# Kernel optimization log

Hardware: AMD Instinct MI355X
Metric: run time of the kernel (lower is better)

Reference implementation:

```python
import jax, jax.numpy as jnp
import numpy as np

L, HID, NH, NKV, HD, INTER = 16, 960, 15, 5, 64, 2560
VOCAB, NV, NT, PRE, SD = 49152, 192, 48, 241, 32
THETA, EPS, B = 100000.0, 1e-5, 16
GROUPS = NH // NKV


def setup_inputs() -> dict:
    key = jax.random.key(0)
    ks = jax.random.split(key, 20)
    s = 0.02
    rn = lambda k, shp: jax.random.normal(k, shp, jnp.float32) * s
    return {
        'vision_features': jax.random.normal(ks[0], (B, NV, HID), jnp.float32),
        'lang_token_ids': jax.random.randint(ks[1], (B, NT), 0, VOCAB),
        'lang_mask': jnp.ones((B, NT), dtype=bool),
        'state': jax.random.normal(ks[2], (B, SD), jnp.float32),
        'embed': rn(ks[3], (VOCAB, HID)),
        'state_w': rn(ks[4], (SD, HID)),
        'state_b': jnp.zeros((HID,), jnp.float32),
        'Wq': rn(ks[5], (L, HID, NH * HD)),
        'Wk': rn(ks[6], (L, HID, NKV * HD)),
        'Wv': rn(ks[7], (L, HID, NKV * HD)),
        'Wo': rn(ks[8], (L, NH * HD, HID)),
        'Wg': rn(ks[9], (L, HID, INTER)),
        'Wu': rn(ks[10], (L, HID, INTER)),
        'Wd': rn(ks[11], (L, INTER, HID)),
        'ln1': jnp.ones((L, HID), jnp.float32),
        'ln2': jnp.ones((L, HID), jnp.float32),
    }


def _rms(x, w):
    var = jnp.mean(jnp.square(x), axis=-1, keepdims=True)
    return x * jax.lax.rsqrt(var + EPS) * w


def _rotate_half(x):
    h = x.shape[-1] // 2
    return jnp.concatenate([-x[..., h:], x[..., :h]], axis=-1)


def _rope_tables(position_ids):
    # position_ids: [B, S] -> cos/sin: [B, S, HD]
    inv_freq = 1.0 / (THETA ** (jnp.arange(0, HD, 2, dtype=jnp.float32) / HD))
    freqs = position_ids.astype(jnp.float32)[..., None] * inv_freq  # [B,S,HD/2]
    emb = jnp.concatenate([freqs, freqs], axis=-1)
    return jnp.cos(emb), jnp.sin(emb)


def _apply_rope(x, cos, sin):
    # x: [B,S,H,D]; cos/sin: [B,S,D]
    return x * cos[:, :, None, :] + _rotate_half(x) * sin[:, :, None, :]


def _attention(q, k, v, mask2d):
    # q: [B,S,NH,HD]; k,v: [B,S,NKV,HD]; mask2d: [B,S,S] bool (query i, key j)
    kx = jnp.repeat(k, GROUPS, axis=2)  # GQA expand -> [B,S,NH,HD]
    vx = jnp.repeat(v, GROUPS, axis=2)
    scores = jnp.einsum('bihd,bjhd->bhij', q, kx) * (HD ** -0.5)
    big_neg = jnp.finfo(jnp.float32).min
    scores = jnp.where(mask2d[:, None, :, :], scores, big_neg)
    probs = jax.nn.softmax(scores, axis=-1)
    out = jnp.einsum('bhij,bjhd->bihd', probs, vx)
    return out.reshape(q.shape[0], q.shape[1], NH * HD)


def reference(vision_features, lang_token_ids, lang_mask, state,
              embed, state_w, state_b, Wq, Wk, Wv, Wo, Wg, Wu, Wd, ln1, ln2):
    lang_emb = embed[lang_token_ids] * jnp.sqrt(jnp.float32(HID))  # [B,NT,HID]
    state_emb = (state @ state_w + state_b)[:, None, :]            # [B,1,HID]
    x = jnp.concatenate([vision_features, lang_emb, state_emb], axis=1)  # [B,PRE,HID]

    pad = jnp.concatenate([jnp.ones((B, NV), bool), lang_mask.astype(bool),
                           jnp.ones((B, 1), bool)], axis=1)  # [B,PRE]
    position_ids = jnp.clip(jnp.cumsum(pad.astype(jnp.int32), axis=1) - 1, 0, None)
    cos, sin = _rope_tables(position_ids)

    att_marks = jnp.zeros((PRE,), jnp.int32).at[NV + NT:].set(1)
    cum = jnp.cumsum(att_marks)
    att2d = cum[None, :] >= cum[:, None]  # [S_q, S_kv]: key cum <= query cum
    pad2d = pad[:, :, None] & pad[:, None, :]
    mask2d = att2d[None, :, :] & pad2d  # [B,S,S]

    def layer(x, w):
        h = _rms(x, w['ln1'])
        S = h.shape[1]
        q = (h @ w['Wq']).reshape(B, S, NH, HD)
        k = (h @ w['Wk']).reshape(B, S, NKV, HD)
        v = (h @ w['Wv']).reshape(B, S, NKV, HD)
        q = _apply_rope(q, cos, sin)
        k = _apply_rope(k, cos, sin)
        a = _attention(q, k, v, mask2d)
        x = x + a @ w['Wo']
        h2 = _rms(x, w['ln2'])
        m = (jax.nn.silu(h2 @ w['Wg']) * (h2 @ w['Wu'])) @ w['Wd']
        return x + m, (k, v)

    weights = {'Wq': Wq, 'Wk': Wk, 'Wv': Wv, 'Wo': Wo,
               'Wg': Wg, 'Wu': Wu, 'Wd': Wd, 'ln1': ln1, 'ln2': ln2}
    _, (keys, values) = jax.lax.scan(layer, x, weights)
    # keys/values: [L, B, PRE, NKV, HD]
    return keys, values
```

## Files before the change

### kernel.cpp

```cpp
#include <hip/hip_runtime.h>
#include <hip/hip_bf16.h>

namespace {

typedef __bf16 bf16_t;
typedef __bf16 bf16x8 __attribute__((ext_vector_type(8)));
typedef __bf16 bf16x4 __attribute__((ext_vector_type(4)));
typedef float f32x4 __attribute__((ext_vector_type(4)));

constexpr int kL     = 16;
constexpr int kHid   = 960;
constexpr int kNH    = 15;
constexpr int kNKV   = 5;
constexpr int kHD    = 64;
constexpr int kInter = 2560;
constexpr int kNV    = 192;
constexpr int kNT    = 48;
constexpr int kPre   = 241;
constexpr int kSD    = 32;
constexpr int kB     = 16;
constexpr int kTok   = kB * kPre;
constexpr int kTokP  = 3968;
constexpr int kQKV   = 1600;
constexpr float kEps = 1e-5f;
constexpr float kSqrtHid = 30.98386677f;

__global__ void build_x_kernel(const float* __restrict__ vision,
                               const int*   __restrict__ tokens,
                               const float* __restrict__ state,
                               const float* __restrict__ embed,
                               const float* __restrict__ sw,
                               const float* __restrict__ sb,
                               float* __restrict__ x) {
  int idx = blockIdx.x * blockDim.x + threadIdx.x;
  if (idx >= kTok * kHid) return;
  int t = idx / kHid, c = idx - t * kHid;
  int b = t / kPre, s = t - b * kPre;
  float v;
  if (s < kNV) {
    v = vision[((size_t)b * kNV + s) * kHid + c];
  } else if (s < kNV + kNT) {
    int tok = tokens[b * kNT + (s - kNV)];
    v = embed[(size_t)tok * kHid + c] * kSqrtHid;
  } else {
    float acc = sb[c];
#pragma unroll
    for (int i = 0; i < kSD; ++i) acc += state[b * kSD + i] * sw[i * kHid + c];
    v = acc;
  }
  x[idx] = v;
}

__global__ void rope_table_kernel(float* __restrict__ cosT, float* __restrict__ sinT) {
  int idx = blockIdx.x * blockDim.x + threadIdx.x;
  if (idx >= kPre * 32) return;
  int s = idx >> 5, fi = idx & 31;
  float inv = __expf(-(2.0f * (float)fi / (float)kHD) * __logf(100000.0f));
  float fr = (float)s * inv;
  cosT[idx] = cosf(fr);
  sinT[idx] = sinf(fr);
}

__device__ void transpose_tile(const float* __restrict__ src, bf16_t* __restrict__ dst,
                               int K, int N, int tile) {
  __shared__ float ts[64][65];
  int ntn = N >> 6;
  int tk = tile / ntn, tn = tile - tk * ntn;
  int t = threadIdx.x;
  int r = t >> 2, c0 = (t & 3) << 4;
  const float* sp = src + (size_t)((tk << 6) + r) * N + (tn << 6) + c0;
  float4 a = ((const float4*)sp)[0];
  float4 b = ((const float4*)sp)[1];
  float4 c = ((const float4*)sp)[2];
  float4 d = ((const float4*)sp)[3];
  ts[r][c0 + 0] = a.x;  ts[r][c0 + 1] = a.y;  ts[r][c0 + 2] = a.z;  ts[r][c0 + 3] = a.w;
  ts[r][c0 + 4] = b.x;  ts[r][c0 + 5] = b.y;  ts[r][c0 + 6] = b.z;  ts[r][c0 + 7] = b.w;
  ts[r][c0 + 8] = c.x;  ts[r][c0 + 9] = c.y;  ts[r][c0 +10] = c.z;  ts[r][c0 +11] = c.w;
  ts[r][c0 +12] = d.x;  ts[r][c0 +13] = d.y;  ts[r][c0 +14] = d.z;  ts[r][c0 +15] = d.w;
  __syncthreads();
  bf16_t* dp = dst + (size_t)((tn << 6) + r) * K + (tk << 6) + c0;
  bf16x8 o0, o1;
#pragma unroll
  for (int i = 0; i < 8; ++i) o0[i] = (bf16_t)ts[c0 + i][r];
#pragma unroll
  for (int i = 0; i < 8; ++i) o1[i] = (bf16_t)ts[c0 + 8 + i][r];
  *(bf16x8*)dp = o0;
  *(bf16x8*)(dp + 8) = o1;
}

__global__ __launch_bounds__(256)
void wconv_kernel(const float* s0, const float* s1, const float* s2, const float* s3,
                  const float* s4, const float* s5, const float* s6,
                  bf16_t* t0, bf16_t* t1, bf16_t* t2, bf16_t* t3,
                  bf16_t* t4, bf16_t* t5, bf16_t* t6) {
  int bid = blockIdx.x;
  if      (bid < 225)  transpose_tile(s0, t0, 960, 960, bid);
  else if (bid < 300)  transpose_tile(s1, t1, 960, 320, bid - 225);
  else if (bid < 375)  transpose_tile(s2, t2, 960, 320, bid - 300);
  else if (bid < 600)  transpose_tile(s3, t3, 960, 960, bid - 375);
  else if (bid < 1200) transpose_tile(s4, t4, 960, 2560, bid - 600);
  else if (bid < 1800) transpose_tile(s5, t5, 960, 2560, bid - 1200);
  else                 transpose_tile(s6, t6, 2560, 960, bid - 1800);
}

__global__ __launch_bounds__(256)
void rmsnorm_bf16_kernel(const float* __restrict__ x, const float* __restrict__ w,
                         bf16_t* __restrict__ h) {
  int t = blockIdx.x;
  int tid = threadIdx.x;
  const float* xr = x + (size_t)t * kHid;
  float4 v = make_float4(0.f, 0.f, 0.f, 0.f);
  if (tid < 240) v = ((const float4*)xr)[tid];
  float ss = v.x * v.x + v.y * v.y + v.z * v.z + v.w * v.w;
#pragma unroll
  for (int off = 32; off; off >>= 1) ss += __shfl_xor(ss, off);
  __shared__ float part[4];
  if ((tid & 63) == 0) part[tid >> 6] = ss;
  __syncthreads();
  float tot = part[0] + part[1] + part[2] + part[3];
  float scale = rsqrtf(tot * (1.f / (float)kHid) + kEps);
  if (tid < 240) {
    float4 wv = ((const float4*)w)[tid];
    bf16x4 o;
    o[0] = (bf16_t)(v.x * scale * wv.x);
    o[1] = (bf16_t)(v.y * scale * wv.y);
    o[2] = (bf16_t)(v.z * scale * wv.z);
    o[3] = (bf16_t)(v.w * scale * wv.w);
    *(bf16x4*)&h[(size_t)t * kHid + tid * 4] = o;
  }
}

template <int MODE>
__global__ __launch_bounds__(256)
void gemm_bf16_kernel(const bf16_t* __restrict__ A, const bf16_t* __restrict__ Bt,
                      const float* __restrict__ src, float* __restrict__ C,
                      int M, int N, int K, int Ncs) {
  constexpr int LDT = 40;
  __shared__ alignas(16) bf16_t As[128 * LDT];
  __shared__ alignas(16) bf16_t Bs[128 * LDT];
  int tid = threadIdx.x;
  int m0 = blockIdx.y * 128, n0 = blockIdx.x * 128;
  int lane = tid & 63, wid = tid >> 6;
  int wr = (wid >> 1) * 64, wc = (wid & 1) * 64;
  int r0 = tid >> 2, c0 = (tid & 3) * 8;

  const bf16_t* ga0 = A + (size_t)(m0 + r0) * K + c0;
  const bf16_t* ga1 = ga0 + (size_t)64 * K;
  const bf16_t* gb0 = Bt + (size_t)(n0 + r0) * K + c0;
  const bf16_t* gb1 = gb0 + (size_t)64 * K;
  bf16_t* wa0 = &As[r0 * LDT + c0];
  bf16_t* wa1 = &As[(r0 + 64) * LDT + c0];
  bf16_t* wb0 = &Bs[r0 * LDT + c0];
  bf16_t* wb1 = &Bs[(r0 + 64) * LDT + c0];

  f32x4 acc[4][4];
#pragma unroll
  for (int m = 0; m < 4; ++m)
#pragma unroll
    for (int n = 0; n < 4; ++n) acc[m][n] = (f32x4){0.f, 0.f, 0.f, 0.f};

  bf16x8 ra0 = *(const bf16x8*)ga0;
  bf16x8 ra1 = *(const bf16x8*)ga1;
  bf16x8 rb0 = *(const bf16x8*)gb0;
  bf16x8 rb1 = *(const bf16x8*)gb1;

  int arow0 = (wr + (lane & 15)) * LDT + (lane >> 4) * 8;
  int brow0 = (wc + (lane & 15)) * LDT + (lane >> 4) * 8;

  for (int k0 = 0;;) {
    __syncthreads();
    *(bf16x8*)wa0 = ra0;  *(bf16x8*)wa1 = ra1;
    *(bf16x8*)wb0 = rb0;  *(bf16x8*)wb1 = rb1;
    __syncthreads();
    k0 += 32;
    if (k0 < K) {
      ra0 = *(const bf16x8*)(ga0 + k0);
      ra1 = *(const bf16x8*)(ga1 + k0);
      rb0 = *(const bf16x8*)(gb0 + k0);
      rb1 = *(const bf16x8*)(gb1 + k0);
    }
    bf16x8 af[4], bfr[4];
#pragma unroll
    for (int m = 0; m < 4; ++m) af[m] = *(const bf16x8*)&As[arow0 + m * 16 * LDT];
#pragma unroll
    for (int n = 0; n < 4; ++n) bfr[n] = *(const bf16x8*)&Bs[brow0 + n * 16 * LDT];
#pragma unroll
    for (int m = 0; m < 4; ++m)
#pragma unroll
      for (int n = 0; n < 4; ++n)
        acc[m][n] = __builtin_amdgcn_mfma_f32_16x16x32_bf16(af[m], bfr[n], acc[m][n], 0, 0, 0);
    if (k0 >= K) break;
  }

  int cr = (lane >> 4) * 4;
  int ccol = lane & 15;
#pragma unroll
  for (int m = 0; m < 4; ++m) {
    int row = m0 + wr + m * 16 + cr;
#pragma unroll
    for (int n = 0; n < 4; ++n) {
      int col = n0 + wc + n * 16 + ccol;
      if (col < N) {
#pragma unroll
        for (int r = 0; r < 4; ++r) {
          int rr = row + r;
          if (rr < M) {
            size_t off = (size_t)rr * Ncs + col;
            float val = acc[m][n][r];
            if (MODE == 1) val += src[off];
            C[off] = val;
          }
        }
      }
    }
  }
}

__global__ __launch_bounds__(256)
void gemm_dual_kernel(const bf16_t* __restrict__ A, const bf16_t* __restrict__ Bg,
                      const bf16_t* __restrict__ Bu, bf16_t* __restrict__ act,
                      int M, int K) {
  constexpr int LDT = 40;
  __shared__ alignas(16) bf16_t As[128 * LDT];
  __shared__ alignas(16) bf16_t Gs[128 * LDT];
  __shared__ alignas(16) bf16_t Us[128 * LDT];
  int tid = threadIdx.x;
  int m0 = blockIdx.y * 128, n0 = blockIdx.x * 128;
  int lane = tid & 63, wid = tid >> 6;
  int wr = (wid >> 1) * 64, wc = (wid & 1) * 64;
  int r0 = tid >> 2, c0 = (tid & 3) * 8;

  const bf16_t* ga0 = A + (size_t)(m0 + r0) * K + c0;
  const bf16_t* ga1 = ga0 + (size_t)64 * K;
  const bf16_t* gg0 = Bg + (size_t)(n0 + r0) * K + c0;
  const bf16_t* gg1 = gg0 + (size_t)64 * K;
  const bf16_t* gu0 = Bu + (size_t)(n0 + r0) * K + c0;
  const bf16_t* gu1 = gu0 + (size_t)64 * K;
  bf16_t* wa0 = &As[r0 * LDT + c0];
  bf16_t* wa1 = &As[(r0 + 64) * LDT + c0];
  bf16_t* wg0 = &Gs[r0 * LDT + c0];
  bf16_t* wg1 = &Gs[(r0 + 64) * LDT + c0];
  bf16_t* wu0 = &Us[r0 * LDT + c0];
  bf16_t* wu1 = &Us[(r0 + 64) * LDT + c0];

  f32x4 accg[4][4], accu[4][4];
#pragma unroll
  for (int m = 0; m < 4; ++m)
#pragma unroll
    for (int n = 0; n < 4; ++n) {
      accg[m][n] = (f32x4){0.f, 0.f, 0.f, 0.f};
      accu[m][n] = (f32x4){0.f, 0.f, 0.f, 0.f};
    }

  bf16x8 ra0 = *(const bf16x8*)ga0;
  bf16x8 ra1 = *(const bf16x8*)ga1;
  bf16x8 rg0 = *(const bf16x8*)gg0;
  bf16x8 rg1 = *(const bf16x8*)gg1;
  bf16x8 ru0 = *(const bf16x8*)gu0;
  bf16x8 ru1 = *(const bf16x8*)gu1;

  int arow0 = (wr + (lane & 15)) * LDT + (lane >> 4) * 8;
  int brow0 = (wc + (lane & 15)) * LDT + (lane >> 4) * 8;

  for (int k0 = 0;;) {
    __syncthreads();
    *(bf16x8*)wa0 = ra0;  *(bf16x8*)wa1 = ra1;
    *(bf16x8*)wg0 = rg0;  *(bf16x8*)wg1 = rg1;
    *(bf16x8*)wu0 = ru0;  *(bf16x8*)wu1 = ru1;
    __syncthreads();
    k0 += 32;
    if (k0 < K) {
      ra0 = *(const bf16x8*)(ga0 + k0);
      ra1 = *(const bf16x8*)(ga1 + k0);
      rg0 = *(const bf16x8*)(gg0 + k0);
      rg1 = *(const bf16x8*)(gg1 + k0);
      ru0 = *(const bf16x8*)(gu0 + k0);
      ru1 = *(const bf16x8*)(gu1 + k0);
    }
    bf16x8 af[4], bfr[4];
#pragma unroll
    for (int m = 0; m < 4; ++m) af[m] = *(const bf16x8*)&As[arow0 + m * 16 * LDT];
#pragma unroll
    for (int n = 0; n < 4; ++n) bfr[n] = *(const bf16x8*)&Gs[brow0 + n * 16 * LDT];
#pragma unroll
    for (int m = 0; m < 4; ++m)
#pragma unroll
      for (int n = 0; n < 4; ++n)
        accg[m][n] = __builtin_amdgcn_mfma_f32_16x16x32_bf16(af[m], bfr[n], accg[m][n], 0, 0, 0);
#pragma unroll
    for (int n = 0; n < 4; ++n) bfr[n] = *(const bf16x8*)&Us[brow0 + n * 16 * LDT];
#pragma unroll
    for (int m = 0; m < 4; ++m)
#pragma unroll
      for (int n = 0; n < 4; ++n)
        accu[m][n] = __builtin_amdgcn_mfma_f32_16x16x32_bf16(af[m], bfr[n], accu[m][n], 0, 0, 0);
    if (k0 >= K) break;
  }

  int cr = (lane >> 4) * 4;
  int ccol = lane & 15;
#pragma unroll
  for (int m = 0; m < 4; ++m) {
    int row = m0 + wr + m * 16 + cr;
#pragma unroll
    for (int n = 0; n < 4; ++n) {
      int col = n0 + wc + n * 16 + ccol;
#pragma unroll
      for (int r = 0; r < 4; ++r) {
        int rr = row + r;
        if (rr < M) {
          float g = accg[m][n][r];
          float u = accu[m][n][r];
          float silu = g / (1.f + __expf(-g));
          act[(size_t)rr * kInter + col] = (bf16_t)(silu * u);
        }
      }
    }
  }
}

__global__ void rope_qkv_kernel(float* __restrict__ qkv, float* __restrict__ kout,
                                float* __restrict__ vout,
                                const float* __restrict__ cosT,
                                const float* __restrict__ sinT) {
  int idx = blockIdx.x * blockDim.x + threadIdx.x;
  constexpr int per_tok = 25 * 32;
  if (idx >= kTok * per_tok) return;
  int t = idx / per_tok, r = idx - t * per_tok;
  int head = r >> 5, d = r & 31;
  int s = t % kPre;
  if (head < 15) {
    float c = cosT[s * 32 + d], sn = sinT[s * 32 + d];
    float* p = qkv + (size_t)t * kQKV + head * kHD + d;
    float x0 = p[0], x1 = p[32];
    p[0]  = x0 * c - x1 * sn;
    p[32] = x1 * c + x0 * sn;
  } else if (head < 20) {
    float c = cosT[s * 32 + d], sn = sinT[s * 32 + d];
    int kh = head - 15;
    float* p = qkv + (size_t)t * kQKV + 960 + kh * kHD + d;
    float x0 = p[0], x1 = p[32];
    float y0 = x0 * c - x1 * sn;
    float y1 = x1 * c + x0 * sn;
    p[0] = y0; p[32] = y1;
    float* po = kout + (size_t)t * 320 + kh * kHD + d;
    po[0] = y0; po[32] = y1;
  } else {
    int vh = head - 20;
    const float* p = qkv + (size_t)t * kQKV + 1280 + vh * kHD + d;
    float* po = vout + (size_t)t * 320 + vh * kHD + d;
    po[0] = p[0]; po[32] = p[32];
  }
}

__global__ __launch_bounds__(256)
void attn_mfma_kernel(const float* __restrict__ qkv, bf16_t* __restrict__ aout) {
  int h = blockIdx.x, b = blockIdx.y;
  int kvh = h / 3;
  constexpr int LDK = 72;
  constexpr int LDV = 264;
  __shared__ alignas(16) bf16_t Ks[256 * LDK];
  __shared__ alignas(16) bf16_t Vt[64 * LDV];
  __shared__ alignas(16) bf16_t Ps[4][16 * LDV];
  const float* base = qkv + (size_t)b * kPre * kQKV;
  int tid = threadIdx.x;
  for (int i = tid; i < 256 * 16; i += 256) {
    int j = i >> 4, c = (i & 15) * 4;
    float4 kv = make_float4(0.f, 0.f, 0.f, 0.f);
    float4 vv = make_float4(0.f, 0.f, 0.f, 0.f);
    if (j < kPre) {
      const float* kp = base + (size_t)j * kQKV + 960 + kvh * 64 + c;
      kv = *(const float4*)kp;
      vv = *(const float4*)(kp + 320);
    }
    bf16x4 k4;
    k4[0] = (bf16_t)kv.x; k4[1] = (bf16_t)kv.y; k4[2] = (bf16_t)kv.z; k4[3] = (bf16_t)kv.w;
    *(bf16x4*)&Ks[j * LDK + c] = k4;
    Vt[(c + 0) * LDV + j] = (bf16_t)vv.x;
    Vt[(c + 1) * LDV + j] = (bf16_t)vv.y;
    Vt[(c + 2) * LDV + j] = (bf16_t)vv.z;
    Vt[(c + 3) * LDV + j] = (bf16_t)vv.w;
  }
  __syncthreads();
  int wid = tid >> 6, lane = tid & 63;
  int lr = lane & 15, lg = lane >> 4;
  bf16_t* myP = &Ps[wid][0];
  for (int qt = wid * 4; qt < wid * 4 + 4; ++qt) {
    int q0 = qt * 16;
    int qrow = q0 + lr; if (qrow > 240) qrow = 240;
    const float* qp = base + (size_t)qrow * kQKV + h * 64 + lg * 8;
    float4 qa = *(const float4*)qp;
    float4 qb = *(const float4*)(qp + 4);
    float4 qc = *(const float4*)(qp + 32);
    float4 qd = *(const float4*)(qp + 36);
    bf16x8 aq0, aq1;
    aq0[0] = (bf16_t)(qa.x * 0.125f); aq0[1] = (bf16_t)(qa.y * 0.125f);
    aq0[2] = (bf16_t)(qa.z * 0.125f); aq0[3] = (bf16_t)(qa.w * 0.125f);
    aq0[4] = (bf16_t)(qb.x * 0.125f); aq0[5] = (bf16_t)(qb.y * 0.125f);
    aq0[6] = (bf16_t)(qb.z * 0.125f); aq0[7] = (bf16_t)(qb.w * 0.125f);
    aq1[0] = (bf16_t)(qc.x * 0.125f); aq1[1] = (bf16_t)(qc.y * 0.125f);
    aq1[2] = (bf16_t)(qc.z * 0.125f); aq1[3] = (bf16_t)(qc.w * 0.125f);
    aq1[4] = (bf16_t)(qd.x * 0.125f); aq1[5] = (bf16_t)(qd.y * 0.125f);
    aq1[6] = (bf16_t)(qd.z * 0.125f); aq1[7] = (bf16_t)(qd.w * 0.125f);
    f32x4 sacc[16];
#pragma unroll
    for (int ct = 0; ct < 16; ++ct) sacc[ct] = (f32x4){0.f, 0.f, 0.f, 0.f};
#pragma unroll
    for (int ct = 0; ct < 16; ++ct) {
      int key = ct * 16 + lr;
      bf16x8 kb0 = *(const bf16x8*)&Ks[key * LDK + lg * 8];
      sacc[ct] = __builtin_amdgcn_mfma_f32_16x16x32_bf16(aq0, kb0, sacc[ct], 0, 0, 0);
      bf16x8 kb1 = *(const bf16x8*)&Ks[key * LDK + 32 + lg * 8];
      sacc[ct] = __builtin_amdgcn_mfma_f32_16x16x32_bf16(aq1, kb1, sacc[ct], 0, 0, 0);
    }
    float rmax[4] = {-1e30f, -1e30f, -1e30f, -1e30f};
#pragma unroll
    for (int ct = 0; ct < 16; ++ct) {
      int j = ct * 16 + lr;
#pragma unroll
      for (int r = 0; r < 4; ++r) {
        int q = q0 + lg * 4 + r;
        bool ok = (q < 240) ? (j < kPre) : (j == 240);
        float s = ok ? sacc[ct][r] : -1e30f;
        sacc[ct][r] = s;
        rmax[r] = fmaxf(rmax[r], s);
      }
    }
#pragma unroll
    for (int off = 8; off; off >>= 1) {
#pragma unroll
      for (int r = 0; r < 4; ++r) rmax[r] = fmaxf(rmax[r], __shfl_xor(rmax[r], off));
    }
    float rsum[4] = {0.f, 0.f, 0.f, 0.f};
#pragma unroll
    for (int ct = 0; ct < 16; ++ct) {
#pragma unroll
      for (int r = 0; r < 4; ++r) {
        float s = sacc[ct][r];
        float e = (s > -1e29f) ? __expf(s - rmax[r]) : 0.f;
        rsum[r] += e;
        myP[(lg * 4 + r) * LDV + ct * 16 + lr] = (bf16_t)e;
      }
    }
#pragma unroll
    for (int off = 8; off; off >>= 1) {
#pragma unroll
      for (int r = 0; r < 4; ++r) rsum[r] += __shfl_xor(rsum[r], off);
    }
    f32x4 oacc[4];
#pragma unroll
    for (int dt = 0; dt < 4; ++dt) oacc[dt] = (f32x4){0.f, 0.f, 0.f, 0.f};
#pragma unroll
    for (int ks = 0; ks < 8; ++ks) {
      bf16x8 pa = *(const bf16x8*)&myP[lr * LDV + ks * 32 + lg * 8];
#pragma unroll
      for (int dt = 0; dt < 4; ++dt) {
        bf16x8 vbf = *(const bf16x8*)&Vt[(dt * 16 + lr) * LDV + ks * 32 + lg * 8];
        oacc[dt] = __builtin_amdgcn_mfma_f32_16x16x32_bf16(pa, vbf, oacc[dt], 0, 0, 0);
      }
    }
    float linv[4];
#pragma unroll
    for (int r = 0; r < 4; ++r) linv[r] = 1.f / rsum[r];
#pragma unroll
    for (int dt = 0; dt < 4; ++dt) {
#pragma unroll
      for (int r = 0; r < 4; ++r) {
        int q = q0 + lg * 4 + r;
        if (q < kPre) {
          aout[((size_t)b * kPre + q) * kHid + h * 64 + dt * 16 + lr] =
              (bf16_t)(oacc[dt][r] * linv[r]);
        }
      }
    }
  }
}

}

extern "C" void kernel_launch(void* const* d_in, const int* in_sizes, int n_in,
                              void* d_out, int out_size, void* d_ws, size_t ws_size,
                              hipStream_t stream) {
  const float* vision = (const float*)d_in[0];
  const int*   tokens = (const int*)d_in[1];
  const float* state = (const float*)d_in[3];
  const float* embed = (const float*)d_in[4];
  const float* sw    = (const float*)d_in[5];
  const float* sb    = (const float*)d_in[6];
  const float* Wq    = (const float*)d_in[7];
  const float* Wk    = (const float*)d_in[8];
  const float* Wv    = (const float*)d_in[9];
  const float* Wo    = (const float*)d_in[10];
  const float* Wg    = (const float*)d_in[11];
  const float* Wu    = (const float*)d_in[12];
  const float* Wd    = (const float*)d_in[13];
  const float* ln1   = (const float*)d_in[14];
  const float* ln2   = (const float*)d_in[15];

  char* w = (char*)d_ws;
  float*  x      = (float*)w;        w += (size_t)kTok * kHid * 4;
  float*  qkv    = (float*)w;        w += (size_t)kTok * kQKV * 4;
  bf16_t* h_bf   = (bf16_t*)w;       w += (size_t)kTokP * kHid * 2;
  bf16_t* a_bf   = (bf16_t*)w;       w += (size_t)kTokP * kHid * 2;
  bf16_t* act_bf = (bf16_t*)w;       w += (size_t)kTokP * kInter * 2;
  bf16_t* wqkv_t = (bf16_t*)w;       w += (size_t)1664 * 960 * 2;
  bf16_t* wo_t   = (bf16_t*)w;       w += (size_t)1024 * 960 * 2;
  bf16_t* wg_t   = (bf16_t*)w;       w += (size_t)2560 * 960 * 2;
  bf16_t* wu_t   = (bf16_t*)w;       w += (size_t)2560 * 960 * 2;
  bf16_t* wd_t   = (bf16_t*)w;       w += (size_t)1024 * 2560 * 2;
  float*  cosT   = (float*)w;        w += (size_t)kPre * 32 * 4;
  float*  sinT   = (float*)w;        w += (size_t)kPre * 32 * 4;

  float* out_k = (float*)d_out;
  float* out_v = out_k + (size_t)kL * kTok * 320;

  build_x_kernel<<<(kTok * kHid + 255) / 256, 256, 0, stream>>>(
      vision, tokens, state, embed, sw, sb, x);
  rope_table_kernel<<<(kPre * 32 + 255) / 256, 256, 0, stream>>>(cosT, sinT);

  for (int l = 0; l < kL; ++l) {
    wconv_kernel<<<2400, 256, 0, stream>>>(
        Wq + (size_t)l * 960 * 960, Wk + (size_t)l * 960 * 320,
        Wv + (size_t)l * 960 * 320, Wo + (size_t)l * 960 * 960,
        Wg + (size_t)l * 960 * 2560, Wu + (size_t)l * 960 * 2560,
        Wd + (size_t)l * 2560 * 960,
        wqkv_t, wqkv_t + (size_t)960 * 960, wqkv_t + (size_t)1280 * 960,
        wo_t, wg_t, wu_t, wd_t);
    rmsnorm_bf16_kernel<<<kTok, 256, 0, stream>>>(x, ln1 + (size_t)l * kHid, h_bf);
    gemm_bf16_kernel<0><<<dim3(13, 31), 256, 0, stream>>>(
        h_bf, wqkv_t, nullptr, qkv, kTok, kQKV, kHid, kQKV);
    rope_qkv_kernel<<<(kTok * 800 + 255) / 256, 256, 0, stream>>>(
        qkv, out_k + (size_t)l * kTok * 320, out_v + (size_t)l * kTok * 320, cosT, sinT);
    attn_mfma_kernel<<<dim3(15, 16), 256, 0, stream>>>(qkv, a_bf);
    gemm_bf16_kernel<1><<<dim3(8, 31), 256, 0, stream>>>(
        a_bf, wo_t, x, x, kTok, kHid, kHid, kHid);
    rmsnorm_bf16_kernel<<<kTok, 256, 0, stream>>>(x, ln2 + (size_t)l * kHid, h_bf);
    gemm_dual_kernel<<<dim3(20, 31), 256, 0, stream>>>(
        h_bf, wg_t, wu_t, act_bf, kTok, kHid);
    gemm_bf16_kernel<1><<<dim3(8, 31), 256, 0, stream>>>(
        act_bf, wd_t, x, x, kTok, kHid, kInter, kHid);
  }
}
```

Measured before the change: 4.246 ms.

## Fuse RoPE into QKV GEMM, batch weight conversion, use direct global-to-LDS loads

Weight transposition and bf16 conversion for all layers now run in a single launch before the layer loop, replacing sixteen per-layer launches. RoPE, the query scale and the K/V output writes move into the QKV GEMM epilogue, which removes the separate rope kernel and stores qkv as bf16 instead of fp32. Attention then reads bf16 directly. All GEMMs switch from register-staged LDS loads to global_load_lds with an unpadded LDS layout. The register prefetch overlap is dropped, and the unpadded layout may cause LDS bank conflicts.

```diff
diff --git a/kernel.cpp b/kernel.cpp
--- a/kernel.cpp
+++ b/kernel.cpp
@@ -24,6 +24,17 @@
 constexpr int kQKV   = 1600;
 constexpr float kEps = 1e-5f;
 constexpr float kSqrtHid = 30.98386677f;
+
+constexpr size_t kWoOff     = (size_t)1664 * 960;
+constexpr size_t kWgOff     = kWoOff + (size_t)1024 * 960;
+constexpr size_t kWuOff     = kWgOff + (size_t)2560 * 960;
+constexpr size_t kWdOff     = kWuOff + (size_t)2560 * 960;
+constexpr size_t kWPerLayer = kWdOff + (size_t)1024 * 2560;
+
+__device__ __forceinline__ void gload16(const bf16_t* g, bf16_t* l) {
+  __builtin_amdgcn_global_load_lds((const __attribute__((address_space(1))) void*)g,
+                                   (__attribute__((address_space(3))) void*)l, 16, 0, 0);
+}
 
 __global__ void build_x_kernel(const float* __restrict__ vision,
                                const int*   __restrict__ tokens,
@@ -89,18 +100,20 @@
 }
 
 __global__ __launch_bounds__(256)
-void wconv_kernel(const float* s0, const float* s1, const float* s2, const float* s3,
-                  const float* s4, const float* s5, const float* s6,
-                  bf16_t* t0, bf16_t* t1, bf16_t* t2, bf16_t* t3,
-                  bf16_t* t4, bf16_t* t5, bf16_t* t6) {
+void wconv_kernel(const float* __restrict__ Wq, const float* __restrict__ Wk,
+                  const float* __restrict__ Wv, const float* __restrict__ Wo,
+                  const float* __restrict__ Wg, const float* __restrict__ Wu,
+                  const float* __restrict__ Wd, bf16_t* __restrict__ wall) {
   int bid = blockIdx.x;
-  if      (bid < 225)  transpose_tile(s0, t0, 960, 960, bid);
-  else if (bid < 300)  transpose_tile(s1, t1, 960, 320, bid - 225);
-  else if (bid < 375)  transpose_tile(s2, t2, 960, 320, bid - 300);
-  else if (bid < 600)  transpose_tile(s3, t3, 960, 960, bid - 375);
-  else if (bid < 1200) transpose_tile(s4, t4, 960, 2560, bid - 600);
-  else if (bid < 1800) transpose_tile(s5, t5, 960, 2560, bid - 1200);
-  else                 transpose_tile(s6, t6, 2560, 960, bid - 1800);
+  int l = bid / 2400, t = bid - l * 2400;
+  bf16_t* wl = wall + (size_t)l * kWPerLayer;
+  if      (t < 225)  transpose_tile(Wq + (size_t)l * 921600, wl, 960, 960, t);
+  else if (t < 300)  transpose_tile(Wk + (size_t)l * 307200, wl + (size_t)960 * 960, 960, 320, t - 225);
+  else if (t < 375)  transpose_tile(Wv + (size_t)l * 307200, wl + (size_t)1280 * 960, 960, 320, t - 300);
+  else if (t < 600)  transpose_tile(Wo + (size_t)l * 921600, wl + kWoOff, 960, 960, t - 375);
+  else if (t < 1200) transpose_tile(Wg + (size_t)l * 2457600, wl + kWgOff, 960, 2560, t - 600);
+  else if (t < 1800) transpose_tile(Wu + (size_t)l * 2457600, wl + kWuOff, 960, 2560, t - 1200);
+  else               transpose_tile(Wd + (size_t)l * 2457600, wl + kWdOff, 2560, 960, t - 1800);
 }
 
 __global__ __launch_bounds__(256)
@@ -130,28 +143,30 @@
   }
 }
 
-template <int MODE>
+
 __global__ __launch_bounds__(256)
-void gemm_bf16_kernel(const bf16_t* __restrict__ A, const bf16_t* __restrict__ Bt,
-                      const float* __restrict__ src, float* __restrict__ C,
-                      int M, int N, int K, int Ncs) {
-  constexpr int LDT = 40;
-  __shared__ alignas(16) bf16_t As[128 * LDT];
-  __shared__ alignas(16) bf16_t Bs[128 * LDT];
+void gemm_qkv_kernel(const bf16_t* __restrict__ A, const bf16_t* __restrict__ Bt,
+                     bf16_t* __restrict__ qkv, float* __restrict__ outk,
+                     float* __restrict__ outv,
+                     const float* __restrict__ cosT, const float* __restrict__ sinT) {
+  constexpr int K = kHid;
+  __shared__ alignas(16) bf16_t As[4096];
+  __shared__ alignas(16) bf16_t Bs[4096];
   int tid = threadIdx.x;
   int m0 = blockIdx.y * 128, n0 = blockIdx.x * 128;
   int lane = tid & 63, wid = tid >> 6;
   int wr = (wid >> 1) * 64, wc = (wid & 1) * 64;
   int r0 = tid >> 2, c0 = (tid & 3) * 8;
-
-  const bf16_t* ga0 = A + (size_t)(m0 + r0) * K + c0;
-  const bf16_t* ga1 = ga0 + (size_t)64 * K;
-  const bf16_t* gb0 = Bt + (size_t)(n0 + r0) * K + c0;
-  const bf16_t* gb1 = gb0 + (size_t)64 * K;
-  bf16_t* wa0 = &As[r0 * LDT + c0];
-  bf16_t* wa1 = &As[(r0 + 64) * LDT + c0];
-  bf16_t* wb0 = &Bs[r0 * LDT + c0];
-  bf16_t* wb1 = &Bs[(r0 + 64) * LDT + c0];
+  int lr = lane & 15, lg = lane >> 4;
+
+  const bf16_t* a0 = A + (size_t)(m0 + r0) * K + c0;
+  const bf16_t* a1 = a0 + (size_t)64 * K;
+  const bf16_t* b0 = Bt + (size_t)(n0 + r0) * K + c0;
+  const bf16_t* b1 = b0 + (size_t)64 * K;
+  bf16_t* la0 = &As[tid * 8];
+  bf16_t* la1 = &As[2048 + tid * 8];
+  bf16_t* lb0 = &Bs[tid * 8];
+  bf16_t* lb1 = &Bs[2048 + tid * 8];
 
   f32x4 acc[4][4];
 #pragma unroll
@@ -159,89 +174,176 @@
 #pragma unroll
     for (int n = 0; n < 4; ++n) acc[m][n] = (f32x4){0.f, 0.f, 0.f, 0.f};
 
-  bf16x8 ra0 = *(const bf16x8*)ga0;
-  bf16x8 ra1 = *(const bf16x8*)ga1;
-  bf16x8 rb0 = *(const bf16x8*)gb0;
-  bf16x8 rb1 = *(const bf16x8*)gb1;
-
-  int arow0 = (wr + (lane & 15)) * LDT + (lane >> 4) * 8;
-  int brow0 = (wc + (lane & 15)) * LDT + (lane >> 4) * 8;
-
-  for (int k0 = 0;;) {
+  int arow0 = (wr + lr) * 32 + lg * 8;
+  int brow0 = (wc + lr) * 32 + lg * 8;
+
+  for (int k0 = 0; k0 < K; k0 += 32) {
     __syncthreads();
-    *(bf16x8*)wa0 = ra0;  *(bf16x8*)wa1 = ra1;
-    *(bf16x8*)wb0 = rb0;  *(bf16x8*)wb1 = rb1;
+    gload16(a0 + k0, la0);
+    gload16(a1 + k0, la1);
+    gload16(b0 + k0, lb0);
+    gload16(b1 + k0, lb1);
     __syncthreads();
-    k0 += 32;
-    if (k0 < K) {
-      ra0 = *(const bf16x8*)(ga0 + k0);
-      ra1 = *(const bf16x8*)(ga1 + k0);
-      rb0 = *(const bf16x8*)(gb0 + k0);
-      rb1 = *(const bf16x8*)(gb1 + k0);
-    }
     bf16x8 af[4], bfr[4];
 #pragma unroll
-    for (int m = 0; m < 4; ++m) af[m] = *(const bf16x8*)&As[arow0 + m * 16 * LDT];
-#pragma unroll
-    for (int n = 0; n < 4; ++n) bfr[n] = *(const bf16x8*)&Bs[brow0 + n * 16 * LDT];
+    for (int m = 0; m < 4; ++m) af[m] = *(const bf16x8*)&As[arow0 + m * 16 * 32];
+#pragma unroll
+    for (int n = 0; n < 4; ++n) bfr[n] = *(const bf16x8*)&Bs[brow0 + n * 16 * 32];
 #pragma unroll
     for (int m = 0; m < 4; ++m)
 #pragma unroll
       for (int n = 0; n < 4; ++n)
         acc[m][n] = __builtin_amdgcn_mfma_f32_16x16x32_bf16(af[m], bfr[n], acc[m][n], 0, 0, 0);
-    if (k0 >= K) break;
-  }
-
-  int cr = (lane >> 4) * 4;
-  int ccol = lane & 15;
-#pragma unroll
-  for (int m = 0; m < 4; ++m) {
-    int row = m0 + wr + m * 16 + cr;
-#pragma unroll
-    for (int n = 0; n < 4; ++n) {
-      int col = n0 + wc + n * 16 + ccol;
-      if (col < N) {
-#pragma unroll
-        for (int r = 0; r < 4; ++r) {
-          int rr = row + r;
-          if (rr < M) {
-            size_t off = (size_t)rr * Ncs + col;
-            float val = acc[m][n][r];
-            if (MODE == 1) val += src[off];
-            C[off] = val;
-          }
+  }
+
+  int cbase = n0 + wc;
+  if (cbase >= kQKV) return;
+  int cr4 = lg * 4;
+  if (cbase < 1280) {
+    bool isQ = cbase < 960;
+    float scale = isQ ? 0.125f : 1.0f;
+#pragma unroll
+    for (int m = 0; m < 4; ++m) {
+      int row = m0 + wr + m * 16 + cr4;
+#pragma unroll
+      for (int r = 0; r < 4; ++r) {
+        int rr = row + r;
+        if (rr >= kTok) continue;
+        int s = rr % kPre;
+        bf16_t* qrow = qkv + (size_t)rr * kQKV + cbase;
+        float* krow = outk + (size_t)rr * 320 + (cbase - 960);
+#pragma unroll
+        for (int n = 0; n < 2; ++n) {
+          int d = n * 16 + lr;
+          float c = cosT[s * 32 + d], sn = sinT[s * 32 + d];
+          float lo = acc[m][n][r], hi = acc[m][n + 2][r];
+          float y0 = lo * c - hi * sn;
+          float y1 = hi * c + lo * sn;
+          qrow[d]      = (bf16_t)(y0 * scale);
+          qrow[d + 32] = (bf16_t)(y1 * scale);
+          if (!isQ) { krow[d] = y0; krow[d + 32] = y1; }
         }
       }
     }
+  } else {
+#pragma unroll
+    for (int m = 0; m < 4; ++m) {
+      int row = m0 + wr + m * 16 + cr4;
+#pragma unroll
+      for (int r = 0; r < 4; ++r) {
+        int rr = row + r;
+        if (rr >= kTok) continue;
+        bf16_t* qrow = qkv + (size_t)rr * kQKV + cbase;
+        float* vrow = outv + (size_t)rr * 320 + (cbase - 1280);
+#pragma unroll
+        for (int n = 0; n < 4; ++n) {
+          int d = n * 16 + lr;
+          float v = acc[m][n][r];
+          qrow[d] = (bf16_t)v;
+          vrow[d] = v;
+        }
+      }
+    }
   }
 }
 
 __global__ __launch_bounds__(256)
-void gemm_dual_kernel(const bf16_t* __restrict__ A, const bf16_t* __restrict__ Bg,
-                      const bf16_t* __restrict__ Bu, bf16_t* __restrict__ act,
-                      int M, int K) {
-  constexpr int LDT = 40;
-  __shared__ alignas(16) bf16_t As[128 * LDT];
-  __shared__ alignas(16) bf16_t Gs[128 * LDT];
-  __shared__ alignas(16) bf16_t Us[128 * LDT];
+void gemm_res_kernel(const bf16_t* __restrict__ A, const bf16_t* __restrict__ Bt,
+                     const float* __restrict__ src, float* __restrict__ C,
+                     int M, int N, int K) {
+  __shared__ alignas(16) bf16_t As[4096];
+  __shared__ alignas(16) bf16_t Bs[4096];
   int tid = threadIdx.x;
   int m0 = blockIdx.y * 128, n0 = blockIdx.x * 128;
   int lane = tid & 63, wid = tid >> 6;
   int wr = (wid >> 1) * 64, wc = (wid & 1) * 64;
   int r0 = tid >> 2, c0 = (tid & 3) * 8;
-
-  const bf16_t* ga0 = A + (size_t)(m0 + r0) * K + c0;
-  const bf16_t* ga1 = ga0 + (size_t)64 * K;
-  const bf16_t* gg0 = Bg + (size_t)(n0 + r0) * K + c0;
-  const bf16_t* gg1 = gg0 + (size_t)64 * K;
-  const bf16_t* gu0 = Bu + (size_t)(n0 + r0) * K + c0;
-  const bf16_t* gu1 = gu0 + (size_t)64 * K;
-  bf16_t* wa0 = &As[r0 * LDT + c0];
-  bf16_t* wa1 = &As[(r0 + 64) * LDT + c0];
-  bf16_t* wg0 = &Gs[r0 * LDT + c0];
-  bf16_t* wg1 = &Gs[(r0 + 64) * LDT + c0];
-  bf16_t* wu0 = &Us[r0 * LDT + c0];
-  bf16_t* wu1 = &Us[(r0 + 64) * LDT + c0];
+  int lr = lane & 15, lg = lane >> 4;
+
+  const bf16_t* a0 = A + (size_t)(m0 + r0) * K + c0;
+  const bf16_t* a1 = a0 + (size_t)64 * K;
+  const bf16_t* b0 = Bt + (size_t)(n0 + r0) * K + c0;
+  const bf16_t* b1 = b0 + (size_t)64 * K;
+  bf16_t* la0 = &As[tid * 8];
+  bf16_t* la1 = &As[2048 + tid * 8];
+  bf16_t* lb0 = &Bs[tid * 8];
+  bf16_t* lb1 = &Bs[2048 + tid * 8];
+
+  f32x4 acc[4][4];
+#pragma unroll
+  for (int m = 0; m < 4; ++m)
+#pragma unroll
+    for (int n = 0; n < 4; ++n) acc[m][n] = (f32x4){0.f, 0.f, 0.f, 0.f};
+
+  int arow0 = (wr + lr) * 32 + lg * 8;
+  int brow0 = (wc + lr) * 32 + lg * 8;
+
+  for (int k0 = 0; k0 < K; k0 += 32) {
+    __syncthreads();
+    gload16(a0 + k0, la0);
+    gload16(a1 + k0, la1);
+    gload16(b0 + k0, lb0);
+    gload16(b1 + k0, lb1);
+    __syncthreads();
+    bf16x8 af[4], bfr[4];
+#pragma unroll
+    for (int m = 0; m < 4; ++m) af[m] = *(const bf16x8*)&As[arow0 + m * 16 * 32];
+#pragma unroll
+    for (int n = 0; n < 4; ++n) bfr[n] = *(const bf16x8*)&Bs[brow0 + n * 16 * 32];
+#pragma unroll
+    for (int m = 0; m < 4; ++m)
+#pragma unroll
+      for (int n = 0; n < 4; ++n)
+        acc[m][n] = __builtin_amdgcn_mfma_f32_16x16x32_bf16(af[m], bfr[n], acc[m][n], 0, 0, 0);
+  }
+
+  int cr4 = lg * 4;
+#pragma unroll
+  for (int m = 0; m < 4; ++m) {
+    int row = m0 + wr + m * 16 + cr4;
+#pragma unroll
+    for (int n = 0; n < 4; ++n) {
+      int col = n0 + wc + n * 16 + lr;
+      if (col < N) {
+#pragma unroll
+        for (int r = 0; r < 4; ++r) {
+          int rr = row + r;
+          if (rr < M) {
+            size_t off = (size_t)rr * N + col;
+            C[off] = src[off] + acc[m][n][r];
+          }
+        }
+      }
+    }
+  }
+}
+
+__global__ __launch_bounds__(256)
+void gemm_dual_kernel(const bf16_t* __restrict__ A, const bf16_t* __restrict__ Bg,
+                      const bf16_t* __restrict__ Bu, bf16_t* __restrict__ act,
+                      int M, int K) {
+  __shared__ alignas(16) bf16_t As[4096];
+  __shared__ alignas(16) bf16_t Gs[4096];
+  __shared__ alignas(16) bf16_t Us[4096];
+  int tid = threadIdx.x;
+  int m0 = blockIdx.y * 128, n0 = blockIdx.x * 128;
+  int lane = tid & 63, wid = tid >> 6;
+  int wr = (wid >> 1) * 64, wc = (wid & 1) * 64;
+  int r0 = tid >> 2, c0 = (tid & 3) * 8;
+  int lr = lane & 15, lg = lane >> 4;
+
+  const bf16_t* a0 = A + (size_t)(m0 + r0) * K + c0;
+  const bf16_t* a1 = a0 + (size_t)64 * K;
+  const bf16_t* g0 = Bg + (size_t)(n0 + r0) * K + c0;
+  const bf16_t* g1 = g0 + (size_t)64 * K;
+  const bf16_t* u0 = Bu + (size_t)(n0 + r0) * K + c0;
+  const bf16_t* u1 = u0 + (size_t)64 * K;
+  bf16_t* la0 = &As[tid * 8];
+  bf16_t* la1 = &As[2048 + tid * 8];
+  bf16_t* lg0 = &Gs[tid * 8];
+  bf16_t* lg1 = &Gs[2048 + tid * 8];
+  bf16_t* lu0 = &Us[tid * 8];
+  bf16_t* lu1 = &Us[2048 + tid * 8];
 
   f32x4 accg[4][4], accu[4][4];
 #pragma unroll
@@ -252,59 +354,44 @@
       accu[m][n] = (f32x4){0.f, 0.f, 0.f, 0.f};
     }
 
-  bf16x8 ra0 = *(const bf16x8*)ga0;
-  bf16x8 ra1 = *(const bf16x8*)ga1;
-  bf16x8 rg0 = *(const bf16x8*)gg0;
-  bf16x8 rg1 = *(const bf16x8*)gg1;
-  bf16x8 ru0 = *(const bf16x8*)gu0;
-  bf16x8 ru1 = *(const bf16x8*)gu1;
-
-  int arow0 = (wr + (lane & 15)) * LDT + (lane >> 4) * 8;
-  int brow0 = (wc + (lane & 15)) * LDT + (lane >> 4) * 8;
-
-  for (int k0 = 0;;) {
+  int arow0 = (wr + lr) * 32 + lg * 8;
+  int brow0 = (wc + lr) * 32 + lg * 8;
+
+  for (int k0 = 0; k0 < K; k0 += 32) {
     __syncthreads();
-    *(bf16x8*)wa0 = ra0;  *(bf16x8*)wa1 = ra1;
-    *(bf16x8*)wg0 = rg0;  *(bf16x8*)wg1 = rg1;
-    *(bf16x8*)wu0 = ru0;  *(bf16x8*)wu1 = ru1;
+    gload16(a0 + k0, la0);
+    gload16(a1 + k0, la1);
+    gload16(g0 + k0, lg0);
+    gload16(g1 + k0, lg1);
+    gload16(u0 + k0, lu0);
+    gload16(u1 + k0, lu1);
     __syncthreads();
-    k0 += 32;
-    if (k0 < K) {
-      ra0 = *(const bf16x8*)(ga0 + k0);
-      ra1 = *(const bf16x8*)(ga1 + k0);
-      rg0 = *(const bf16x8*)(gg0 + k0);
-      rg1 = *(const bf16x8*)(gg1 + k0);
-      ru0 = *(const bf16x8*)(gu0 + k0);
-      ru1 = *(const bf16x8*)(gu1 + k0);
-    }
     bf16x8 af[4], bfr[4];
 #pragma unroll
-    for (int m = 0; m < 4; ++m) af[m] = *(const bf16x8*)&As[arow0 + m * 16 * LDT];
-#pragma unroll
-    for (int n = 0; n < 4; ++n) bfr[n] = *(const bf16x8*)&Gs[brow0 + n * 16 * LDT];
+    for (int m = 0; m < 4; ++m) af[m] = *(const bf16x8*)&As[arow0 + m * 16 * 32];
+#pragma unroll
+    for (int n = 0; n < 4; ++n) bfr[n] = *(const bf16x8*)&Gs[brow0 + n * 16 * 32];
 #pragma unroll
     for (int m = 0; m < 4; ++m)
 #pragma unroll
       for (int n = 0; n < 4; ++n)
         accg[m][n] = __builtin_amdgcn_mfma_f32_16x16x32_bf16(af[m], bfr[n], accg[m][n], 0, 0, 0);
 #pragma unroll
-    for (int n = 0; n < 4; ++n) bfr[n] = *(const bf16x8*)&Us[brow0 + n * 16 * LDT];
+    for (int n = 0; n < 4; ++n) bfr[n] = *(const bf16x8*)&Us[brow0 + n * 16 * 32];
 #pragma unroll
     for (int m = 0; m < 4; ++m)
 #pragma unroll
       for (int n = 0; n < 4; ++n)
         accu[m][n] = __builtin_amdgcn_mfma_f32_16x16x32_bf16(af[m], bfr[n], accu[m][n], 0, 0, 0);
-    if (k0 >= K) break;
-  }
-
-  int cr = (lane >> 4) * 4;
-  int ccol = lane & 15;
+  }
+
+  int cr4 = lg * 4;
 #pragma unroll
   for (int m = 0; m < 4; ++m) {
-    int row = m0 + wr + m * 16 + cr;
+    int row = m0 + wr + m * 16 + cr4;
 #pragma unroll
     for (int n = 0; n < 4; ++n) {
-      int col = n0 + wc + n * 16 + ccol;
+      int col = n0 + wc + n * 16 + lr;
 #pragma unroll
       for (int r = 0; r < 4; ++r) {
         int rr = row + r;
@@ -319,42 +406,8 @@
   }
 }
 
-__global__ void rope_qkv_kernel(float* __restrict__ qkv, float* __restrict__ kout,
-                                float* __restrict__ vout,
-                                const float* __restrict__ cosT,
-                                const float* __restrict__ sinT) {
-  int idx = blockIdx.x * blockDim.x + threadIdx.x;
-  constexpr int per_tok = 25 * 32;
-  if (idx >= kTok * per_tok) return;
-  int t = idx / per_tok, r = idx - t * per_tok;
-  int head = r >> 5, d = r & 31;
-  int s = t % kPre;
-  if (head < 15) {
-    float c = cosT[s * 32 + d], sn = sinT[s * 32 + d];
-    float* p = qkv + (size_t)t * kQKV + head * kHD + d;
-    float x0 = p[0], x1 = p[32];
-    p[0]  = x0 * c - x1 * sn;
-    p[32] = x1 * c + x0 * sn;
-  } else if (head < 20) {
-    float c = cosT[s * 32 + d], sn = sinT[s * 32 + d];
-    int kh = head - 15;
-    float* p = qkv + (size_t)t * kQKV + 960 + kh * kHD + d;
-    float x0 = p[0], x1 = p[32];
-    float y0 = x0 * c - x1 * sn;
-    float y1 = x1 * c + x0 * sn;
-    p[0] = y0; p[32] = y1;
-    float* po = kout + (size_t)t * 320 + kh * kHD + d;
-    po[0] = y0; po[32] = y1;
-  } else {
-    int vh = head - 20;
-    const float* p = qkv + (size_t)t * kQKV + 1280 + vh * kHD + d;
-    float* po = vout + (size_t)t * 320 + vh * kHD + d;
-    po[0] = p[0]; po[32] = p[32];
-  }
-}
-
 __global__ __launch_bounds__(256)
-void attn_mfma_kernel(const float* __restrict__ qkv, bf16_t* __restrict__ aout) {
+void attn_mfma_kernel(const bf16_t* __restrict__ qkv, bf16_t* __restrict__ aout) {
   int h = blockIdx.x, b = blockIdx.y;
   int kvh = h / 3;
   constexpr int LDK = 72;
@@ -362,24 +415,21 @@
   __shared__ alignas(16) bf16_t Ks[256 * LDK];
   __shared__ alignas(16) bf16_t Vt[64 * LDV];
   __shared__ alignas(16) bf16_t Ps[4][16 * LDV];
-  const float* base = qkv + (size_t)b * kPre * kQKV;
+  const bf16_t* base = qkv + (size_t)b * kPre * kQKV;
   int tid = threadIdx.x;
-  for (int i = tid; i < 256 * 16; i += 256) {
-    int j = i >> 4, c = (i & 15) * 4;
-    float4 kv = make_float4(0.f, 0.f, 0.f, 0.f);
-    float4 vv = make_float4(0.f, 0.f, 0.f, 0.f);
+  for (int i = tid; i < 2048; i += 256) {
+    int j = i >> 3, c = (i & 7) * 8;
+    bf16x8 k8, v8;
     if (j < kPre) {
-      const float* kp = base + (size_t)j * kQKV + 960 + kvh * 64 + c;
-      kv = *(const float4*)kp;
-      vv = *(const float4*)(kp + 320);
-    }
-    bf16x4 k4;
-    k4[0] = (bf16_t)kv.x; k4[1] = (bf16_t)kv.y; k4[2] = (bf16_t)kv.z; k4[3] = (bf16_t)kv.w;
-    *(bf16x4*)&Ks[j * LDK + c] = k4;
-    Vt[(c + 0) * LDV + j] = (bf16_t)vv.x;
-    Vt[(c + 1) * LDV + j] = (bf16_t)vv.y;
-    Vt[(c + 2) * LDV + j] = (bf16_t)vv.z;
-    Vt[(c + 3) * LDV + j] = (bf16_t)vv.w;
+      k8 = *(const bf16x8*)(base + (size_t)j * kQKV + 960 + kvh * 64 + c);
+      v8 = *(const bf16x8*)(base + (size_t)j * kQKV + 1280 + kvh * 64 + c);
+    } else {
+#pragma unroll
+      for (int e = 0; e < 8; ++e) { k8[e] = (bf16_t)0.f; v8[e] = (bf16_t)0.f; }
+    }
+    *(bf16x8*)&Ks[j * LDK + c] = k8;
+#pragma unroll
+    for (int e = 0; e < 8; ++e) Vt[(c + e) * LDV + j] = v8[e];
   }
   __syncthreads();
   int wid = tid >> 6, lane = tid & 63;
@@ -388,20 +438,9 @@
   for (int qt = wid * 4; qt < wid * 4 + 4; ++qt) {
     int q0 = qt * 16;
     int qrow = q0 + lr; if (qrow > 240) qrow = 240;
-    const float* qp = base + (size_t)qrow * kQKV + h * 64 + lg * 8;
-    float4 qa = *(const float4*)qp;
-    float4 qb = *(const float4*)(qp + 4);
-    float4 qc = *(const float4*)(qp + 32);
-    float4 qd = *(const float4*)(qp + 36);
-    bf16x8 aq0, aq1;
-    aq0[0] = (bf16_t)(qa.x * 0.125f); aq0[1] = (bf16_t)(qa.y * 0.125f);
-    aq0[2] = (bf16_t)(qa.z * 0.125f); aq0[3] = (bf16_t)(qa.w * 0.125f);
-    aq0[4] = (bf16_t)(qb.x * 0.125f); aq0[5] = (bf16_t)(qb.y * 0.125f);
-    aq0[6] = (bf16_t)(qb.z * 0.125f); aq0[7] = (bf16_t)(qb.w * 0.125f);
-    aq1[0] = (bf16_t)(qc.x * 0.125f); aq1[1] = (bf16_t)(qc.y * 0.125f);
-    aq1[2] = (bf16_t)(qc.z * 0.125f); aq1[3] = (bf16_t)(qc.w * 0.125f);
-    aq1[4] = (bf16_t)(qd.x * 0.125f); aq1[5] = (bf16_t)(qd.y * 0.125f);
-    aq1[6] = (bf16_t)(qd.z * 0.125f); aq1[7] = (bf16_t)(qd.w * 0.125f);
+    const bf16_t* qp = base + (size_t)qrow * kQKV + h * 64 + lg * 8;
+    bf16x8 aq0 = *(const bf16x8*)qp;
+    bf16x8 aq1 = *(const bf16x8*)(qp + 32);
     f32x4 sacc[16];
 #pragma unroll
     for (int ct = 0; ct < 16; ++ct) sacc[ct] = (f32x4){0.f, 0.f, 0.f, 0.f};
@@ -498,18 +537,14 @@
   const float* ln2   = (const float*)d_in[15];
 
   char* w = (char*)d_ws;
-  float*  x      = (float*)w;        w += (size_t)kTok * kHid * 4;
-  float*  qkv    = (float*)w;        w += (size_t)kTok * kQKV * 4;
-  bf16_t* h_bf   = (bf16_t*)w;       w += (size_t)kTokP * kHid * 2;
-  bf16_t* a_bf   = (bf16_t*)w;       w += (size_t)kTokP * kHid * 2;
-  bf16_t* act_bf = (bf16_t*)w;       w += (size_t)kTokP * kInter * 2;
-  bf16_t* wqkv_t = (bf16_t*)w;       w += (size_t)1664 * 960 * 2;
-  bf16_t* wo_t   = (bf16_t*)w;       w += (size_t)1024 * 960 * 2;
-  bf16_t* wg_t   = (bf16_t*)w;       w += (size_t)2560 * 960 * 2;
-  bf16_t* wu_t   = (bf16_t*)w;       w += (size_t)2560 * 960 * 2;
-  bf16_t* wd_t   = (bf16_t*)w;       w += (size_t)1024 * 2560 * 2;
-  float*  cosT   = (float*)w;        w += (size_t)kPre * 32 * 4;
-  float*  sinT   = (float*)w;        w += (size_t)kPre * 32 * 4;
+  float*  x      = (float*)w;   w += (size_t)kTok * kHid * 4;
+  bf16_t* qkv    = (bf16_t*)w;  w += (size_t)kTok * kQKV * 2;
+  bf16_t* h_bf   = (bf16_t*)w;  w += (size_t)kTokP * kHid * 2;
+  bf16_t* a_bf   = (bf16_t*)w;  w += (size_t)kTokP * kHid * 2;
+  bf16_t* act_bf = (bf16_t*)w;  w += (size_t)kTokP * kInter * 2;
+  bf16_t* wall   = (bf16_t*)w;  w += kWPerLayer * kL * 2;
+  float*  cosT   = (float*)w;   w += (size_t)kPre * 32 * 4;
+  float*  sinT   = (float*)w;   w += (size_t)kPre * 32 * 4;
 
   float* out_k = (float*)d_out;
   float* out_v = out_k + (size_t)kL * kTok * 320;
@@ -517,27 +552,21 @@
   build_x_kernel<<<(kTok * kHid + 255) / 256, 256, 0, stream>>>(
       vision, tokens, state, embed, sw, sb, x);
   rope_table_kernel<<<(kPre * 32 + 255) / 256, 256, 0, stream>>>(cosT, sinT);
+  wconv_kernel<<<2400 * kL, 256, 0, stream>>>(Wq, Wk, Wv, Wo, Wg, Wu, Wd, wall);
 
   for (int l = 0; l < kL; ++l) {
-    wconv_kernel<<<2400, 256, 0, stream>>>(
-        Wq + (size_t)l * 960 * 960, Wk + (size_t)l * 960 * 320,
-        Wv + (size_t)l * 960 * 320, Wo + (size_t)l * 960 * 960,
-        Wg + (size_t)l * 960 * 2560, Wu + (size_t)l * 960 * 2560,
-        Wd + (size_t)l * 2560 * 960,
-        wqkv_t, wqkv_t + (size_t)960 * 960, wqkv_t + (size_t)1280 * 960,
-        wo_t, wg_t, wu_t, wd_t);
+    bf16_t* wl = wall + (size_t)l * kWPerLayer;
     rmsnorm_bf16_kernel<<<kTok, 256, 0, stream>>>(x, ln1 + (size_t)l * kHid, h_bf);
-    gemm_bf16_kernel<0><<<dim3(13, 31), 256, 0, stream>>>(
-        h_bf, wqkv_t, nullptr, qkv, kTok, kQKV, kHid, kQKV);
-    rope_qkv_kernel<<<(kTok * 800 + 255) / 256, 256, 0, stream>>>(
-        qkv, out_k + (size_t)l * kTok * 320, out_v + (size_t)l * kTok * 320, cosT, sinT);
+    gemm_qkv_kernel<<<dim3(13, 31), 256, 0, stream>>>(
+        h_bf, wl, qkv, out_k + (size_t)l * kTok * 320, out_v + (size_t)l * kTok * 320,
+        cosT, sinT);
     attn_mfma_kernel<<<dim3(15, 16), 256, 0, stream>>>(qkv, a_bf);
-    gemm_bf16_kernel<1><<<dim3(8, 31), 256, 0, stream>>>(
-        a_bf, wo_t, x, x, kTok, kHid, kHid, kHid);
+    gemm_res_kernel<<<dim3(8, 31), 256, 0, stream>>>(
+        a_bf, wl + kWoOff, x, x, kTok, kHid, kHid);
     rmsnorm_bf16_kernel<<<kTok, 256, 0, stream>>>(x, ln2 + (size_t)l * kHid, h_bf);
     gemm_dual_kernel<<<dim3(20, 31), 256, 0, stream>>>(
-        h_bf, wg_t, wu_t, act_bf, kTok, kHid);
-    gemm_bf16_kernel<1><<<dim3(8, 31), 256, 0, stream>>>(
-        act_bf, wd_t, x, x, kTok, kHid, kInter, kHid);
-  }
-}
+        h_bf, wl + kWgOff, wl + kWuOff, act_bf, kTok, kHid);
+    gemm_res_kernel<<<dim3(8, 31), 256, 0, stream>>>(
+        act_bf, wl + kWdOff, x, x, kTok, kHid, kInter);
+  }
+}
```

Result: slower. 5.266 ms (+24.0%).
